# Kernel optimization log

Measured on AMD Instinct MI355X. Metric: run time of the kernel, lower is better.

Reference implementation:

```python
import jax, jax.numpy as jnp
import numpy as np

M, K, N = 8192, 4096, 4096
INT8_MAX = 127.0


def setup_inputs() -> dict:
    key = jax.random.key(0)
    k1, k2, k3, k4 = jax.random.split(key, 4)
    inp = jax.random.normal(k1, (M, K), dtype=jnp.float32)
    # int8 weight [out_features, in_features]
    weight = jax.random.randint(k2, (N, K), -128, 128, dtype=jnp.int32).astype(jnp.int8)
    # per-output-channel dequant scale
    weight_scale = jax.random.uniform(k3, (N,), dtype=jnp.float32, minval=1e-3, maxval=1e-2)
    bias = jax.random.normal(k4, (N,), dtype=jnp.float32) * 0.01
    return {"input": inp, "weight": weight, "weight_scale": weight_scale, "bias": bias}


def reference(input, weight, weight_scale, bias):
    # Dynamic per-token symmetric int8 quantization (scaled_int8_quant with
    # scale=None, azp=None, symmetric=True): scale_a = max|x| / 127 per row.
    absmax = jnp.max(jnp.abs(input), axis=-1, keepdims=True)  # [M, 1]
    scale_a = jnp.where(absmax > 0, absmax / INT8_MAX, jnp.float32(1.0))
    q = jnp.clip(jnp.round(input / scale_a), -128, 127).astype(jnp.int8)  # [M, K]
    # and per-column (weight_scale) dequant, plus bias, in input dtype.
    acc = jnp.matmul(q.astype(jnp.int32), weight.T.astype(jnp.int32))  # [M, N] int32
    out = acc.astype(jnp.float32) * scale_a * weight_scale[None, :] + bias[None, :]
    return out.astype(input.dtype)
```

## Files before the change

### kernel.cpp

```cpp
#include <hip/hip_runtime.h>
#include <cstdint>

typedef __attribute__((ext_vector_type(4))) int int32x4;
typedef __attribute__((ext_vector_type(16))) int int32x16;

#define GLOBAL_AS __attribute__((address_space(1)))
#define LDS_AS    __attribute__((address_space(3)))

__global__ __launch_bounds__(256) void pack_w(
    const int* __restrict__ w32, uint32_t* __restrict__ w8_as_u32)
{
    const size_t i = (size_t)blockIdx.x * 256 + threadIdx.x;
    const int4 v = ((const int4*)w32)[i];
    w8_as_u32[i] = (v.x & 0xff) | ((v.y & 0xff) << 8) |
                   ((v.z & 0xff) << 16) | ((uint32_t)(v.w & 0xff) << 24);
}

__global__ __launch_bounds__(256) void quant_rows(
    const float* __restrict__ in, int8_t* __restrict__ q,
    float* __restrict__ sa, int K)
{
    const int row = blockIdx.x;
    const float4* rp = (const float4*)(in + (size_t)row * K);
    const int t = threadIdx.x;

    float amax = 0.f;
    float4 v[4];
#pragma unroll
    for (int i = 0; i < 4; ++i) {
        v[i] = rp[t + (i << 8)];
        amax = fmaxf(amax,
               fmaxf(fmaxf(fabsf(v[i].x), fabsf(v[i].y)),
                     fmaxf(fabsf(v[i].z), fabsf(v[i].w))));
    }

#pragma unroll
    for (int off = 32; off; off >>= 1)
        amax = fmaxf(amax, __shfl_xor(amax, off));
    __shared__ float smax[4];
    if ((t & 63) == 0) smax[t >> 6] = amax;
    __syncthreads();
    amax = fmaxf(fmaxf(smax[0], smax[1]), fmaxf(smax[2], smax[3]));

    const float scale = (amax > 0.f) ? (amax / 127.f) : 1.f;
    if (t == 0) sa[row] = scale;
    const float rs = 1.f / scale;

    int* qrow = (int*)(q + (size_t)row * K);
#pragma unroll
    for (int i = 0; i < 4; ++i) {
        int a = __float2int_rn(v[i].x * rs);
        int b = __float2int_rn(v[i].y * rs);
        int c = __float2int_rn(v[i].z * rs);
        int d = __float2int_rn(v[i].w * rs);
        a = max(-128, min(127, a));
        b = max(-128, min(127, b));
        c = max(-128, min(127, c));
        d = max(-128, min(127, d));
        qrow[t + (i << 8)] = (a & 0xff) | ((b & 0xff) << 8) |
                             ((c & 0xff) << 16) | ((d & 0xff) << 24);
    }
}

__device__ __forceinline__ void async_load16(const int8_t* g, int8_t* lds) {
    __builtin_amdgcn_global_load_lds((const GLOBAL_AS char*)g,
                                     (LDS_AS char*)lds, 16, 0, 0);
}

__global__ __launch_bounds__(256, 1) void w8a8_gemm(
    const int8_t* __restrict__ Aq, const int8_t* __restrict__ W,
    const float* __restrict__ sa, const float* __restrict__ wsc,
    const float* __restrict__ bias, float* __restrict__ out,
    int M, int N, int K)
{
    __shared__ int8_t lds[2 * 65536];

    const int NB = N >> 8;
    const int nwg = gridDim.x;
    const int cpx = nwg >> 3;
    const int wg = (blockIdx.x & 7) * cpx + (blockIdx.x >> 3);
    const int bm = wg / NB, bn = wg % NB;

    const int t = threadIdx.x;
    const int lane = t & 63, wid = t >> 6;
    const int wr = wid >> 1, wc = wid & 1;
    const int l31 = lane & 31, h = lane >> 5;

    const int srow = ((t >> 7) << 5) + (t & 31);
    const int scol = ((((t >> 6) & 1) * 2 + ((t >> 5) & 1)) << 4);
    const int8_t* gA = Aq + ((size_t)bm * 256 + srow) * (size_t)K + scol;
    const int8_t* gB = W  + ((size_t)bn * 256 + srow) * (size_t)K + scol;
    const size_t rstep = (size_t)64 * K;
    const size_t hstep = (size_t)128 * K;
    int8_t* ldsw = &lds[t * 16];

    auto stage_group = [&](int slot, int kbyte) {
#pragma unroll
        for (int c = 0; c < 8; ++c) {
            const int sub = c & 3;
            const int kt = c >> 2;
            const int8_t* s0 = (sub < 2 ? gA : gB) +
                               (size_t)(sub & 1) * hstep + kbyte + kt * 64;
            int8_t* d0 = ldsw + slot * 65536 + (sub >= 2 ? 32768 : 0) +
                         kt * 16384 + (sub & 1) * 8192;
            async_load16(s0, d0);
            async_load16(s0 + rstep, d0 + 4096);
        }
    };

    const int aoff = wr * 8192 + lane * 16;
    const int boff = 32768 + wc * 8192 + lane * 16;

    int32x16 acc[4][4];
#pragma unroll
    for (int m = 0; m < 4; ++m)
#pragma unroll
        for (int n = 0; n < 4; ++n)
#pragma unroll
            for (int rgi = 0; rgi < 16; ++rgi)
                acc[m][n][rgi] = 0;

    const int NG = K >> 7;

    stage_group(0, 0);
    asm volatile("s_waitcnt vmcnt(0)" ::: "memory");
    asm volatile("s_barrier" ::: "memory");

    for (int g = 0; g < NG; ++g) {
        const int rbase = (g & 1) * 65536;

        if (g + 1 < NG) stage_group((g + 1) & 1, (g + 1) << 7);

#pragma unroll
        for (int kt = 0; kt < 2; ++kt) {
            const int tb = rbase + kt * 16384;
            int32x4 a0[4], b0[4], a1[4], b1[4];
#pragma unroll
            for (int m = 0; m < 4; ++m) {
                a0[m] = *(const int32x4*)&lds[tb + aoff + m * 2048];
                a1[m] = *(const int32x4*)&lds[tb + aoff + m * 2048 + 1024];
            }
#pragma unroll
            for (int n = 0; n < 4; ++n) {
                b0[n] = *(const int32x4*)&lds[tb + boff + n * 2048];
                b1[n] = *(const int32x4*)&lds[tb + boff + n * 2048 + 1024];
            }
#pragma unroll
            for (int m = 0; m < 4; ++m)
#pragma unroll
                for (int n = 0; n < 4; ++n)
                    acc[m][n] = __builtin_amdgcn_mfma_i32_32x32x32_i8(
                        a0[m], b0[n], acc[m][n], 0, 0, 0);
#pragma unroll
            for (int m = 0; m < 4; ++m)
#pragma unroll
                for (int n = 0; n < 4; ++n)
                    acc[m][n] = __builtin_amdgcn_mfma_i32_32x32x32_i8(
                        a1[m], b1[n], acc[m][n], 0, 0, 0);
        }

        asm volatile("s_waitcnt vmcnt(0)" ::: "memory");
        asm volatile("s_barrier" ::: "memory");
    }

    const int col0 = bn * 256 + wc * 128 + l31;
    const int row00 = bm * 256 + wr * 128 + 4 * h;

#pragma unroll
    for (int m = 0; m < 4; ++m) {
        float sv[16];
#pragma unroll
        for (int rgi = 0; rgi < 16; ++rgi)
            sv[rgi] = sa[row00 + m * 32 + (rgi & 3) + 8 * (rgi >> 2)];
#pragma unroll
        for (int n = 0; n < 4; ++n) {
            const int col = col0 + n * 32;
            const float wn = wsc[col];
            const float bb = bias[col];
#pragma unroll
            for (int rgi = 0; rgi < 16; ++rgi) {
                const int row = row00 + m * 32 + (rgi & 3) + 8 * (rgi >> 2);
                out[(size_t)row * N + col] =
                    (float)acc[m][n][rgi] * sv[rgi] * wn + bb;
            }
        }
    }
}

extern "C" void kernel_launch(void* const* d_in, const int* in_sizes, int n_in,
                              void* d_out, int out_size, void* d_ws, size_t ws_size,
                              hipStream_t stream) {
    const float* inp  = (const float*)d_in[0];
    const int*   w32  = (const int*)d_in[1];
    const float* wsc  = (const float*)d_in[2];
    const float* bias = (const float*)d_in[3];
    float* out = (float*)d_out;

    const int N = in_sizes[2];
    const int K = in_sizes[1] / N;
    const int M = in_sizes[0] / K;

    int8_t* q  = (int8_t*)d_ws;
    float*  sa = (float*)((char*)d_ws + (size_t)M * K);
    int8_t* w8 = (int8_t*)((char*)d_ws + (size_t)M * K + (size_t)M * 4 + 256);

    const size_t nw4 = ((size_t)N * K) / 4;
    pack_w<<<(int)(nw4 / 256), 256, 0, stream>>>(w32, (uint32_t*)w8);

    quant_rows<<<M, 256, 0, stream>>>(inp, q, sa, K);

    const int nwg = (M / 256) * (N / 256);
    w8a8_gemm<<<nwg, 256, 0, stream>>>(q, w8, sa, wsc, bias, out, M, N, K);
}
```

Before: 243.9 us.

## Use four-stage LDS ring with register double-buffered fragments in int8 GEMM

The GEMM main loop moves from a 2-slot buffer of 128-deep K groups to a 4-slot ring of 64-deep K tiles, with loads issued three tiles ahead and partial vmcnt waits instead of draining all loads each iteration. LDS fragments for the next tile are read into a second register set while MFMAs run on the current one, so LDS reads overlap compute. This doubles fragment registers, which raises register pressure and could cause spills, and it relies on a single barrier per tile to guard slot reuse.

```diff
diff --git a/kernel.cpp b/kernel.cpp
--- a/kernel.cpp
+++ b/kernel.cpp
@@ -73,7 +73,7 @@
     const float* __restrict__ bias, float* __restrict__ out,
     int M, int N, int K)
 {
-    __shared__ int8_t lds[2 * 65536];
+    __shared__ int8_t lds[4 * 32768];
 
     const int NB = N >> 8;
     const int nwg = gridDim.x;
@@ -86,30 +86,39 @@
     const int wr = wid >> 1, wc = wid & 1;
     const int l31 = lane & 31, h = lane >> 5;
 
-    const int srow = ((t >> 7) << 5) + (t & 31);
+    const int srow = ((t >> 7) & 1) * 32 + (t & 31);
     const int scol = ((((t >> 6) & 1) * 2 + ((t >> 5) & 1)) << 4);
     const int8_t* gA = Aq + ((size_t)bm * 256 + srow) * (size_t)K + scol;
     const int8_t* gB = W  + ((size_t)bn * 256 + srow) * (size_t)K + scol;
-    const size_t rstep = (size_t)64 * K;
-    const size_t hstep = (size_t)128 * K;
+    const size_t cstep = (size_t)64 * K;
     int8_t* ldsw = &lds[t * 16];
 
-    auto stage_group = [&](int slot, int kbyte) {
-#pragma unroll
-        for (int c = 0; c < 8; ++c) {
-            const int sub = c & 3;
-            const int kt = c >> 2;
-            const int8_t* s0 = (sub < 2 ? gA : gB) +
-                               (size_t)(sub & 1) * hstep + kbyte + kt * 64;
-            int8_t* d0 = ldsw + slot * 65536 + (sub >= 2 ? 32768 : 0) +
-                         kt * 16384 + (sub & 1) * 8192;
-            async_load16(s0, d0);
-            async_load16(s0 + rstep, d0 + 4096);
+    auto stage_tile = [&](int slot, int kbyte) {
+        int8_t* d = ldsw + slot * 32768;
+#pragma unroll
+        for (int c = 0; c < 4; ++c) {
+            async_load16(gA + c * cstep + kbyte, d + c * 4096);
+            async_load16(gB + c * cstep + kbyte, d + 16384 + c * 4096);
         }
     };
 
     const int aoff = wr * 8192 + lane * 16;
-    const int boff = 32768 + wc * 8192 + lane * 16;
+    const int boff = 16384 + wc * 8192 + lane * 16;
+
+    auto read_frags = [&](int slot, int32x4 (&A0)[4], int32x4 (&A1)[4],
+                          int32x4 (&B0)[4], int32x4 (&B1)[4]) {
+        const int tb = slot * 32768;
+#pragma unroll
+        for (int m = 0; m < 4; ++m) {
+            A0[m] = *(const int32x4*)&lds[tb + aoff + m * 2048];
+            A1[m] = *(const int32x4*)&lds[tb + aoff + m * 2048 + 1024];
+        }
+#pragma unroll
+        for (int n = 0; n < 4; ++n) {
+            B0[n] = *(const int32x4*)&lds[tb + boff + n * 2048];
+            B1[n] = *(const int32x4*)&lds[tb + boff + n * 2048 + 1024];
+        }
+    };
 
     int32x16 acc[4][4];
 #pragma unroll
@@ -120,48 +129,47 @@
             for (int rgi = 0; rgi < 16; ++rgi)
                 acc[m][n][rgi] = 0;
 
-    const int NG = K >> 7;
-
-    stage_group(0, 0);
-    asm volatile("s_waitcnt vmcnt(0)" ::: "memory");
+    const int NT = K >> 6;
+
+    int32x4 xa0[4], xa1[4], xb0[4], xb1[4];
+    int32x4 ya0[4], ya1[4], yb0[4], yb1[4];
+
+    stage_tile(0, 0);
+    stage_tile(1, 64);
+    stage_tile(2, 128);
+    asm volatile("s_waitcnt vmcnt(8)" ::: "memory");
     asm volatile("s_barrier" ::: "memory");
-
-    for (int g = 0; g < NG; ++g) {
-        const int rbase = (g & 1) * 65536;
-
-        if (g + 1 < NG) stage_group((g + 1) & 1, (g + 1) << 7);
-
-#pragma unroll
-        for (int kt = 0; kt < 2; ++kt) {
-            const int tb = rbase + kt * 16384;
-            int32x4 a0[4], b0[4], a1[4], b1[4];
-#pragma unroll
-            for (int m = 0; m < 4; ++m) {
-                a0[m] = *(const int32x4*)&lds[tb + aoff + m * 2048];
-                a1[m] = *(const int32x4*)&lds[tb + aoff + m * 2048 + 1024];
-            }
-#pragma unroll
-            for (int n = 0; n < 4; ++n) {
-                b0[n] = *(const int32x4*)&lds[tb + boff + n * 2048];
-                b1[n] = *(const int32x4*)&lds[tb + boff + n * 2048 + 1024];
-            }
-#pragma unroll
-            for (int m = 0; m < 4; ++m)
-#pragma unroll
-                for (int n = 0; n < 4; ++n)
-                    acc[m][n] = __builtin_amdgcn_mfma_i32_32x32x32_i8(
-                        a0[m], b0[n], acc[m][n], 0, 0, 0);
-#pragma unroll
-            for (int m = 0; m < 4; ++m)
-#pragma unroll
-                for (int n = 0; n < 4; ++n)
-                    acc[m][n] = __builtin_amdgcn_mfma_i32_32x32x32_i8(
-                        a1[m], b1[n], acc[m][n], 0, 0, 0);
-        }
-
-        asm volatile("s_waitcnt vmcnt(0)" ::: "memory");
-        asm volatile("s_barrier" ::: "memory");
-    }
+    read_frags(0, xa0, xa1, xb0, xb1);
+
+#define ITER_BODY(G, CA0, CA1, CB0, CB1, NA0, NA1, NB0, NB1)                   \
+    {                                                                          \
+        const int g_ = (G);                                                    \
+        if (g_ + 1 < NT) read_frags((g_ + 1) & 3, NA0, NA1, NB0, NB1);         \
+        if (g_ + 3 < NT) stage_tile((g_ + 3) & 3, (g_ + 3) << 6);              \
+        _Pragma("unroll")                                                      \
+        for (int m = 0; m < 4; ++m)                                            \
+            _Pragma("unroll")                                                  \
+            for (int n = 0; n < 4; ++n)                                        \
+                acc[m][n] = __builtin_amdgcn_mfma_i32_32x32x32_i8(             \
+                    CA0[m], CB0[n], acc[m][n], 0, 0, 0);                       \
+        _Pragma("unroll")                                                      \
+        for (int m = 0; m < 4; ++m)                                            \
+            _Pragma("unroll")                                                  \
+            for (int n = 0; n < 4; ++n)                                        \
+                acc[m][n] = __builtin_amdgcn_mfma_i32_32x32x32_i8(             \
+                    CA1[m], CB1[n], acc[m][n], 0, 0, 0);                       \
+        if (g_ + 3 < NT)                                                       \
+            asm volatile("s_waitcnt vmcnt(8)" ::: "memory");                   \
+        else                                                                   \
+            asm volatile("s_waitcnt vmcnt(0)" ::: "memory");                   \
+        asm volatile("s_barrier" ::: "memory");                                \
+    }
+
+    for (int g = 0; g < NT; g += 2) {
+        ITER_BODY(g,     xa0, xa1, xb0, xb1, ya0, ya1, yb0, yb1);
+        ITER_BODY(g + 1, ya0, ya1, yb0, yb1, xa0, xa1, xb0, xb1);
+    }
+#undef ITER_BODY
 
     const int col0 = bn * 256 + wc * 128 + l31;
     const int row00 = bm * 256 + wr * 128 + 4 * h;
```

After: 214.1 us. 1.14x faster.
